# Performance work log

Hardware: AMD Instinct MI355X
Metric: run time of the kernel (lower is better)

## Reference

```python
import jax, jax.numpy as jnp
import numpy as np

NEG_INF = -1e16


def setup_inputs() -> dict:
    key = jax.random.key(0)
    k1, k2, k3 = jax.random.split(key, 3)
    B, N, C, D = 8, 4096, 64, 64
    inputs = jax.random.normal(k1, (B, N, C), dtype=jnp.float32)
    graph = jax.random.randint(k2, (N, N), 0, 2, dtype=jnp.int32)
    # xavier_uniform for Linear weight [D, C]
    limit = float(np.sqrt(6.0 / (C + D)))
    W = jax.random.uniform(k3, (D, C), dtype=jnp.float32, minval=-limit, maxval=limit)
    b = jnp.zeros((D,), dtype=jnp.float32)
    return {"inputs": inputs, "graph": graph, "W": W, "b": b}


def reference(inputs, graph, W, b):
    # h = W(inputs): [B, N, D]
    h = jnp.einsum('bnc,dc->bnd', inputs, W)
    # dense pairwise scores: [B, N, N]
    scores = jnp.einsum('bnd,bmd->bnm', h, h)
    # mask non-edges (graph broadcasts over batch)
    scores = jnp.where(graph[None, :, :] == 0, NEG_INF, scores)
    attention = jax.nn.softmax(scores, axis=2)
    out = jnp.einsum('bnm,bmd->bnd', attention, h) + b
    return out
```

## Files before the change

kernel.cpp:

```cpp
#include <hip/hip_runtime.h>
#include <stdint.h>

typedef _Float16 f16x8 __attribute__((ext_vector_type(8)));
typedef __fp16 half2_t __attribute__((ext_vector_type(2)));
typedef float f32x4 __attribute__((ext_vector_type(4)));

#define LOG2E 1.44269504088896340736f
#define NEGINF (-1e16f)

constexpr int kN = 4096;
constexpr int kD = 64;
constexpr int kB = 8;

__global__ __launch_bounds__(256) void hproj_kernel(const float* __restrict__ x,
                                                    const float* __restrict__ W,
                                                    _Float16* __restrict__ hout,
                                                    _Float16* __restrict__ hTout)
{
    __shared__ float Wt[64][64];
    __shared__ float xs[64][65];

    const int tid = threadIdx.x;
    const int r   = tid >> 2;
    const int c0  = (tid & 3) * 16;

    #pragma unroll
    for (int j = 0; j < 16; j += 4) {
        const float4 v = *(const float4*)(W + r * 64 + c0 + j);
        Wt[c0 + j + 0][r] = v.x;
        Wt[c0 + j + 1][r] = v.y;
        Wt[c0 + j + 2][r] = v.z;
        Wt[c0 + j + 3][r] = v.w;
    }
    const long rowbase = (long)blockIdx.x * 64;
    #pragma unroll
    for (int j = 0; j < 16; j += 4) {
        const float4 v = *(const float4*)(x + (rowbase + r) * 64 + c0 + j);
        xs[r][c0 + j + 0] = v.x;
        xs[r][c0 + j + 1] = v.y;
        xs[r][c0 + j + 2] = v.z;
        xs[r][c0 + j + 3] = v.w;
    }
    __syncthreads();

    const int d0 = (tid & 3) * 16;
    f32x4 acc[4] = {{0.f,0.f,0.f,0.f},{0.f,0.f,0.f,0.f},{0.f,0.f,0.f,0.f},{0.f,0.f,0.f,0.f}};
    #pragma unroll 4
    for (int c = 0; c < 64; ++c) {
        const float xv = xs[r][c];
        const f32x4* wrow = (const f32x4*)&Wt[c][d0];
        #pragma unroll
        for (int k = 0; k < 4; ++k) acc[k] += wrow[k] * xv;
    }
    f16x8 o0, o1;
    #pragma unroll
    for (int j = 0; j < 8; ++j) {
        o0[j] = (_Float16)acc[j >> 2][j & 3];
        o1[j] = (_Float16)acc[2 + (j >> 2)][j & 3];
    }
    *(f16x8*)(hout + (rowbase + r) * 64 + d0)     = o0;
    *(f16x8*)(hout + (rowbase + r) * 64 + d0 + 8) = o1;

    const int bb = blockIdx.x >> 6;
    const int n  = (int)(rowbase + r) & (kN - 1);
    _Float16* hTb = hTout + (long)bb * kD * kN + n;
    #pragma unroll
    for (int j = 0; j < 8; ++j) {
        hTb[(long)(d0 + j) * kN]     = o0[j];
        hTb[(long)(d0 + 8 + j) * kN] = o1[j];
    }
}

__global__ __launch_bounds__(256) void bitpack_kernel(const int* __restrict__ g,
                                                      uint32_t* __restrict__ mw)
{
    const long w = (long)blockIdx.x * 256 + threadIdx.x;
    const int4* p = (const int4*)(g + w * 32);
    uint32_t bits = 0;
    #pragma unroll
    for (int j = 0; j < 8; ++j) {
        const int4 v = p[j];
        bits |= (uint32_t)(v.x != 0) << (j * 4 + 0);
        bits |= (uint32_t)(v.y != 0) << (j * 4 + 1);
        bits |= (uint32_t)(v.z != 0) << (j * 4 + 2);
        bits |= (uint32_t)(v.w != 0) << (j * 4 + 3);
    }
    mw[w] = bits;
}

__global__ __launch_bounds__(256) void masktr_kernel(const uint32_t* __restrict__ mw,
                                                     uint64_t* __restrict__ wmout)
{
    const int tid  = threadIdx.x;
    const int wv   = tid >> 6;
    const int lane = tid & 63;
    const int ll   = lane & 15;
    const int lg   = lane >> 4;
    const int pair = blockIdx.x * 4 + wv;
    const int q16  = pair >> 6;
    const int kv64 = pair & 63;

    const uint2 u = *(const uint2*)(mw + (long)(q16 * 16 + ll) * 128 + kv64 * 2);

    uint64_t Wb[16];
    #pragma unroll
    for (int s = 0; s < 16; ++s) {
        const int t = s >> 2, rr = s & 3;
        const uint32_t word = (t >= 2) ? u.y : u.x;
        const int pos = 8 * lg + 4 * (t & 1) + rr;
        Wb[s] = __ballot(((word >> pos) & 1u) != 0);
    }

    const int s = lane;
    uint64_t a0 = (s & 1) ? Wb[1]  : Wb[0];
    uint64_t a1 = (s & 1) ? Wb[3]  : Wb[2];
    uint64_t a2 = (s & 1) ? Wb[5]  : Wb[4];
    uint64_t a3 = (s & 1) ? Wb[7]  : Wb[6];
    uint64_t a4 = (s & 1) ? Wb[9]  : Wb[8];
    uint64_t a5 = (s & 1) ? Wb[11] : Wb[10];
    uint64_t a6 = (s & 1) ? Wb[13] : Wb[12];
    uint64_t a7 = (s & 1) ? Wb[15] : Wb[14];
    uint64_t b0 = (s & 2) ? a1 : a0;
    uint64_t b1 = (s & 2) ? a3 : a2;
    uint64_t b2 = (s & 2) ? a5 : a4;
    uint64_t b3 = (s & 2) ? a7 : a6;
    uint64_t c0 = (s & 4) ? b1 : b0;
    uint64_t c1 = (s & 4) ? b3 : b2;
    uint64_t v  = (s & 8) ? c1 : c0;
    if (lane < 16) wmout[(long)pair * 16 + lane] = v;
}

__global__ __launch_bounds__(256) void attn_kernel(const _Float16* __restrict__ h,
                                                   const _Float16* __restrict__ hT,
                                                   const uint64_t* __restrict__ wmask,
                                                   const float* __restrict__ bias,
                                                   float* __restrict__ outp,
                                                   float* __restrict__ pO,
                                                   float* __restrict__ pml,
                                                   int kvlen)
{
    __shared__ alignas(16) char Kl[2][8192];
    __shared__ alignas(16) char Vt[2][8192];

    const int b     = blockIdx.y;
    const int split = blockIdx.z;
    const int q0    = blockIdx.x * 64;
    const int tid   = threadIdx.x;
    const int wave  = tid >> 6;
    const int lane  = tid & 63;
    const int lg    = lane >> 4;
    const int ll    = lane & 15;

    const _Float16* hb  = h  + (long)b * kN * kD;
    const _Float16* hTb = hT + (long)b * kD * kN;
    const int kv_base = split * kvlen;
    const int NT      = kvlen / 64;

    const int q = q0 + wave * 16 + ll;
    const f16x8 qf0 = *(const f16x8*)(hb + q * 64 + lg * 8);
    const f16x8 qf1 = *(const f16x8*)(hb + q * 64 + 32 + lg * 8);

    f16x8 vone;
    {
        const _Float16 o = (ll == 0) ? (_Float16)1.0f : (_Float16)0.0f;
        #pragma unroll
        for (int j = 0; j < 8; ++j) vone[j] = o;
    }

    f32x4 Oacc[4] = {{0.f,0.f,0.f,0.f},{0.f,0.f,0.f,0.f},{0.f,0.f,0.f,0.f},{0.f,0.f,0.f,0.f}};
    f32x4 Oacc4 = {0.f, 0.f, 0.f, 0.f};
    float m_run = NEGINF;
    float mm = NEGINF * LOG2E;
    float negv = NEGINF;

    const int sr = tid >> 2;
    const int sc = (tid & 3) * 16;
    const int srp = (sr & 0x23) | ((sr & 0x18) >> 1) | ((sr & 0x4) << 2);

    const int kwA = srp * 128 + ((sc * 2)      ^ ((srp & 7) << 4));
    const int kwB = srp * 128 + ((sc * 2 + 16) ^ ((srp & 7) << 4));
    const int vwA = sr  * 128 + ((sc * 2)      ^ ((sr  & 7) << 4));
    const int vwB = sr  * 128 + ((sc * 2 + 16) ^ ((sr  & 7) << 4));
    const int rb0 = ll * 128 + (((lg * 16))      ^ ((ll & 7) << 4));
    const int rb1 = ll * 128 + (((64 + lg * 16)) ^ ((ll & 7) << 4));

    char* const KB = (char*)Kl;
    char* const VB = (char*)Vt;

    const _Float16* gK = hb  + (long)(kv_base + sr) * 64 + sc;
    const _Float16* gV = hTb + (long)sr * kN + kv_base + sc;

    const int wuni = __builtin_amdgcn_readfirstlane(wave);
    const uint64_t* __restrict__ wmp =
        wmask + ((long)(blockIdx.x * 4 + wuni) * 64 + (kv_base >> 6)) * 16;

    uint64_t wmA[16], wmB[16];
    {
        const f16x8 a0 = *(const f16x8*)(gK);
        const f16x8 a1 = *(const f16x8*)(gK + 8);
        const f16x8 b0 = *(const f16x8*)(gV);
        const f16x8 b1 = *(const f16x8*)(gV + 8);
        *(f16x8*)(KB + kwA) = a0;  *(f16x8*)(KB + kwB) = a1;
        *(f16x8*)(VB + vwA) = b0;  *(f16x8*)(VB + vwB) = b1;
        gK += 64 * 64;  gV += 64;
        #pragma unroll
        for (int s = 0; s < 16; ++s) wmA[s] = wmp[s];
    }

#define TILE_BODY(WMC, WMN, IT, CB, NB)                                          \
    do {                                                                         \
        const int it_ = (IT);                                                    \
        f16x8 nk0{}, nk1{}, nv0{}, nv1{};                                        \
        if (it_ + 1 < NT) {                                                      \
            nk0 = *(const f16x8*)(gK);                                           \
            nk1 = *(const f16x8*)(gK + 8);                                       \
            nv0 = *(const f16x8*)(gV);                                           \
            nv1 = *(const f16x8*)(gV + 8);                                       \
            gK += 64 * 64;  gV += 64;                                            \
            _Pragma("unroll")                                                    \
            for (int s5 = 0; s5 < 16; ++s5) WMN[s5] = wmp[(long)(it_+1)*16 + s5];\
        }                                                                        \
        __syncthreads();                                                         \
        f32x4 S[4];                                                              \
        _Pragma("unroll")                                                        \
        for (int t = 0; t < 4; ++t) {                                            \
            const f16x8 k0 = *(const f16x8*)(KB + (CB) + rb0 + t * 2048);        \
            const f16x8 k1 = *(const f16x8*)(KB + (CB) + rb1 + t * 2048);        \
            f32x4 s = {0.f, 0.f, 0.f, 0.f};                                      \
            s = __builtin_amdgcn_mfma_f32_16x16x32_f16(k0, qf0, s, 0, 0, 0);     \
            s = __builtin_amdgcn_mfma_f32_16x16x32_f16(k1, qf1, s, 0, 0, 0);     \
            S[t] = s;                                                            \
        }                                                                        \
        if (it_ + 1 < NT) {                                                      \
            *(f16x8*)(KB + (NB) + kwA) = nk0;  *(f16x8*)(KB + (NB) + kwB) = nk1; \
            *(f16x8*)(VB + (NB) + vwA) = nv0;  *(f16x8*)(VB + (NB) + vwB) = nv1; \
        }                                                                        \
        _Pragma("unroll")                                                        \
        for (int t = 0; t < 4; ++t) {                                            \
            _Pragma("unroll")                                                    \
            for (int rr = 0; rr < 4; ++rr) {                                     \
                float sv = S[t][rr];                                             \
                asm("v_cndmask_b32 %0, %1, %2, %3"                               \
                    : "=v"(sv) : "v"(negv), "v"(sv), "s"(WMC[t * 4 + rr]));      \
                S[t][rr] = sv;                                                   \
            }                                                                    \
        }                                                                        \
        float mx0 = fmaxf(fmaxf(S[0][0], S[0][1]), fmaxf(S[0][2], S[0][3]));     \
        float mx1 = fmaxf(fmaxf(S[1][0], S[1][1]), fmaxf(S[1][2], S[1][3]));     \
        float mx2 = fmaxf(fmaxf(S[2][0], S[2][1]), fmaxf(S[2][2], S[2][3]));     \
        float mx3 = fmaxf(fmaxf(S[3][0], S[3][1]), fmaxf(S[3][2], S[3][3]));     \
        float mloc = fmaxf(fmaxf(mx0, mx1), fmaxf(mx2, mx3));                    \
        mloc = fmaxf(mloc, __shfl_xor(mloc, 16));                                \
        mloc = fmaxf(mloc, __shfl_xor(mloc, 32));                                \
        if (__any(mloc > m_run + 8.f)) {                                         \
            const float mnew = fmaxf(m_run, mloc);                               \
            const float scl  = __builtin_amdgcn_exp2f((m_run - mnew) * LOG2E);   \
            m_run = mnew;                                                        \
            mm    = mnew * LOG2E;                                                \
            _Pragma("unroll")                                                    \
            for (int dt = 0; dt < 4; ++dt) Oacc[dt] *= scl;                      \
            Oacc4 *= scl;                                                        \
        }                                                                        \
        _Pragma("unroll")                                                        \
        for (int t = 0; t < 4; ++t) {                                            \
            _Pragma("unroll")                                                    \
            for (int rr = 0; rr < 4; ++rr)                                       \
                S[t][rr] = __builtin_amdgcn_exp2f(fmaf(S[t][rr], LOG2E, -mm));   \
        }                                                                        \
        union PF { half2_t hh[4]; f16x8 v; };                                    \
        PF pf1, pf2;                                                             \
        pf1.hh[0] = __builtin_amdgcn_cvt_pkrtz(S[0][0], S[0][1]);                \
        pf1.hh[1] = __builtin_amdgcn_cvt_pkrtz(S[0][2], S[0][3]);                \
        pf1.hh[2] = __builtin_amdgcn_cvt_pkrtz(S[1][0], S[1][1]);                \
        pf1.hh[3] = __builtin_amdgcn_cvt_pkrtz(S[1][2], S[1][3]);                \
        pf2.hh[0] = __builtin_amdgcn_cvt_pkrtz(S[2][0], S[2][1]);                \
        pf2.hh[1] = __builtin_amdgcn_cvt_pkrtz(S[2][2], S[2][3]);                \
        pf2.hh[2] = __builtin_amdgcn_cvt_pkrtz(S[3][0], S[3][1]);                \
        pf2.hh[3] = __builtin_amdgcn_cvt_pkrtz(S[3][2], S[3][3]);                \
        _Pragma("unroll")                                                        \
        for (int dt = 0; dt < 4; ++dt) {                                         \
            const f16x8 v0 = *(const f16x8*)(VB + (CB) + rb0 + dt * 2048);       \
            const f16x8 v1 = *(const f16x8*)(VB + (CB) + rb1 + dt * 2048);       \
            Oacc[dt] = __builtin_amdgcn_mfma_f32_16x16x32_f16(v0, pf1.v, Oacc[dt], 0, 0, 0); \
            Oacc[dt] = __builtin_amdgcn_mfma_f32_16x16x32_f16(v1, pf2.v, Oacc[dt], 0, 0, 0); \
        }                                                                        \
        Oacc4 = __builtin_amdgcn_mfma_f32_16x16x32_f16(vone, pf1.v, Oacc4, 0, 0, 0); \
        Oacc4 = __builtin_amdgcn_mfma_f32_16x16x32_f16(vone, pf2.v, Oacc4, 0, 0, 0); \
    } while (0)

    for (int ith = 0; ith < NT; ith += 2) {
        TILE_BODY(wmA, wmB, ith,     0,    8192);
        TILE_BODY(wmB, wmA, ith + 1, 8192, 0);
    }
#undef TILE_BODY

    const float lsum = __shfl(Oacc4[0], ll, 64);

    if (outp != nullptr) {
        const float inv = 1.0f / lsum;
        #pragma unroll
        for (int dt = 0; dt < 4; ++dt) {
            const int dbase = dt * 16 + lg * 4;
            const f32x4 bv = *(const f32x4*)(bias + dbase);
            f32x4 o;
            #pragma unroll
            for (int rr = 0; rr < 4; ++rr) o[rr] = Oacc[dt][rr] * inv + bv[rr];
            *(f32x4*)(outp + ((long)b * kN + q) * 64 + dbase) = o;
        }
    } else {
        const long srow = (long)split * kB * kN + (long)b * kN + q;
        #pragma unroll
        for (int dt = 0; dt < 4; ++dt) {
            const int dbase = dt * 16 + lg * 4;
            *(f32x4*)(pO + srow * 64 + dbase) = Oacc[dt];
        }
        if (lane < 16) {
            pml[srow * 2 + 0] = m_run;
            pml[srow * 2 + 1] = lsum;
        }
    }
}

__global__ __launch_bounds__(256) void combine_kernel(const float* __restrict__ pO,
                                                      const float* __restrict__ pml,
                                                      const float* __restrict__ bias,
                                                      float* __restrict__ outp,
                                                      int ks)
{
    const long idx = (long)blockIdx.x * 256 + threadIdx.x;
    const long row = idx >> 4;
    const int  d4  = (int)(idx & 15) * 4;

    float M = NEGINF;
    for (int s = 0; s < ks; ++s)
        M = fmaxf(M, pml[((long)s * kB * kN + row) * 2]);

    float L = 0.f;
    f32x4 acc = {0.f, 0.f, 0.f, 0.f};
    for (int s = 0; s < ks; ++s) {
        const long srow = (long)s * kB * kN + row;
        const float m = pml[srow * 2 + 0];
        const float l = pml[srow * 2 + 1];
        const float w = __builtin_amdgcn_exp2f((m - M) * LOG2E);
        L += l * w;
        const f32x4 o = *(const f32x4*)(pO + srow * 64 + d4);
        acc += o * w;
    }
    const float invL = (L > 0.f) ? (1.0f / L) : 0.f;
    const f32x4 bv = *(const f32x4*)(bias + d4);
    *(f32x4*)(outp + row * 64 + d4) = acc * invL + bv;
}

extern "C" void kernel_launch(void* const* d_in, const int* in_sizes, int n_in,
                              void* d_out, int out_size, void* d_ws, size_t ws_size,
                              hipStream_t stream) {
    const float*  x     = (const float*)d_in[0];
    const int*    graph = (const int*)d_in[1];
    const float*  W     = (const float*)d_in[2];
    const float*  bias  = (const float*)d_in[3];
    float*        outp  = (float*)d_out;

    char* ws = (char*)d_ws;
    _Float16* hptr  = (_Float16*)ws;
    uint32_t* mwptr = (uint32_t*)(ws + (4u << 20));
    _Float16* hTptr = (_Float16*)(ws + (6u << 20));
    uint64_t* wmptr = (uint64_t*)(ws + (10u << 20));

    int ks = 1;
    if      (ws_size >= ((size_t)46 << 20)) ks = 4;
    else if (ws_size >= ((size_t)30 << 20)) ks = 2;

    float* pO  = (float*)(ws + (12u << 20));
    float* pml = (float*)(ws + (12u << 20) + (size_t)ks * (8u << 20));

    hproj_kernel<<<dim3(kB * kN / 64), dim3(256), 0, stream>>>(x, W, hptr, hTptr);
    bitpack_kernel<<<dim3(kN * (kN / 32) / 256), dim3(256), 0, stream>>>(graph, mwptr);
    masktr_kernel<<<dim3(256 * 64 / 4), dim3(256), 0, stream>>>(mwptr, wmptr);

    if (ks == 1) {
        attn_kernel<<<dim3(kN / 64, kB, 1), dim3(256), 0, stream>>>(
            hptr, hTptr, wmptr, bias, outp, nullptr, nullptr, kN);
    } else {
        attn_kernel<<<dim3(kN / 64, kB, ks), dim3(256), 0, stream>>>(
            hptr, hTptr, wmptr, bias, nullptr, pO, pml, kN / ks);
        combine_kernel<<<dim3(kB * kN * 16 / 256), dim3(256), 0, stream>>>(
            pO, pml, bias, outp, ks);
    }
}
```

Baseline: 99.12 us.

## Share KV tiles across 8 waves per block and coalesce transposed h writes

The attention kernel now runs 512 threads (8 waves) per block and covers 128 queries, so each K/V tile staged in LDS is reused by twice as many query rows. Each thread now loads half as many fragments per tile. Separately, the projection kernel transposes h through shared memory, so the hT stores become 16-byte vector writes instead of scattered 2-byte stores. In exchange the grid has fewer, larger blocks, which may lower occupancy or hurt load balance, and the split-k grid shrinks.

New measurement: 90.64 us. 8.6% less time.

```diff
diff --git a/kernel.cpp b/kernel.cpp
--- a/kernel.cpp
+++ b/kernel.cpp
@@ -19,6 +19,7 @@
 {
     __shared__ float Wt[64][64];
     __shared__ float xs[64][65];
+    __shared__ _Float16 ht[64][68];
 
     const int tid = threadIdx.x;
     const int r   = tid >> 2;
@@ -61,14 +62,26 @@
     *(f16x8*)(hout + (rowbase + r) * 64 + d0)     = o0;
     *(f16x8*)(hout + (rowbase + r) * 64 + d0 + 8) = o1;
 
+    #pragma unroll
+    for (int j = 0; j < 8; ++j) {
+        ht[r][d0 + j]     = o0[j];
+        ht[r][d0 + 8 + j] = o1[j];
+    }
+    __syncthreads();
+
     const int bb = blockIdx.x >> 6;
-    const int n  = (int)(rowbase + r) & (kN - 1);
-    _Float16* hTb = hTout + (long)bb * kD * kN + n;
+    const int n0 = (int)(rowbase & (kN - 1));
+    const int dr = tid >> 2;
+    const int c4 = (tid & 3) * 16;
+    f16x8 t0, t1;
     #pragma unroll
     for (int j = 0; j < 8; ++j) {
-        hTb[(long)(d0 + j) * kN]     = o0[j];
-        hTb[(long)(d0 + 8 + j) * kN] = o1[j];
-    }
+        t0[j] = ht[c4 + j][dr];
+        t1[j] = ht[c4 + 8 + j][dr];
+    }
+    _Float16* dst = hTout + (long)bb * kD * kN + (long)dr * kN + n0 + c4;
+    *(f16x8*)(dst)     = t0;
+    *(f16x8*)(dst + 8) = t1;
 }
 
 __global__ __launch_bounds__(256) void bitpack_kernel(const int* __restrict__ g,
@@ -130,7 +143,7 @@
     if (lane < 16) wmout[(long)pair * 16 + lane] = v;
 }
 
-__global__ __launch_bounds__(256) void attn_kernel(const _Float16* __restrict__ h,
+__global__ __launch_bounds__(512) void attn_kernel(const _Float16* __restrict__ h,
                                                    const _Float16* __restrict__ hT,
                                                    const uint64_t* __restrict__ wmask,
                                                    const float* __restrict__ bias,
@@ -144,7 +157,7 @@
 
     const int b     = blockIdx.y;
     const int split = blockIdx.z;
-    const int q0    = blockIdx.x * 64;
+    const int q0    = blockIdx.x * 128;
     const int tid   = threadIdx.x;
     const int wave  = tid >> 6;
     const int lane  = tid & 63;
@@ -173,35 +186,31 @@
     float mm = NEGINF * LOG2E;
     float negv = NEGINF;
 
-    const int sr = tid >> 2;
-    const int sc = (tid & 3) * 16;
+    const int sr  = tid >> 3;
+    const int sc8 = (tid & 7) * 8;
     const int srp = (sr & 0x23) | ((sr & 0x18) >> 1) | ((sr & 0x4) << 2);
 
-    const int kwA = srp * 128 + ((sc * 2)      ^ ((srp & 7) << 4));
-    const int kwB = srp * 128 + ((sc * 2 + 16) ^ ((srp & 7) << 4));
-    const int vwA = sr  * 128 + ((sc * 2)      ^ ((sr  & 7) << 4));
-    const int vwB = sr  * 128 + ((sc * 2 + 16) ^ ((sr  & 7) << 4));
+    const int kw = srp * 128 + ((sc8 * 2) ^ ((srp & 7) << 4));
+    const int vw = sr  * 128 + ((sc8 * 2) ^ ((sr  & 7) << 4));
     const int rb0 = ll * 128 + (((lg * 16))      ^ ((ll & 7) << 4));
     const int rb1 = ll * 128 + (((64 + lg * 16)) ^ ((ll & 7) << 4));
 
     char* const KB = (char*)Kl;
     char* const VB = (char*)Vt;
 
-    const _Float16* gK = hb  + (long)(kv_base + sr) * 64 + sc;
-    const _Float16* gV = hTb + (long)sr * kN + kv_base + sc;
+    const _Float16* gK = hb  + (long)(kv_base + sr) * 64 + sc8;
+    const _Float16* gV = hTb + (long)sr * kN + kv_base + sc8;
 
     const int wuni = __builtin_amdgcn_readfirstlane(wave);
     const uint64_t* __restrict__ wmp =
-        wmask + ((long)(blockIdx.x * 4 + wuni) * 64 + (kv_base >> 6)) * 16;
+        wmask + ((long)(blockIdx.x * 8 + wuni) * 64 + (kv_base >> 6)) * 16;
 
     uint64_t wmA[16], wmB[16];
     {
         const f16x8 a0 = *(const f16x8*)(gK);
-        const f16x8 a1 = *(const f16x8*)(gK + 8);
         const f16x8 b0 = *(const f16x8*)(gV);
-        const f16x8 b1 = *(const f16x8*)(gV + 8);
-        *(f16x8*)(KB + kwA) = a0;  *(f16x8*)(KB + kwB) = a1;
-        *(f16x8*)(VB + vwA) = b0;  *(f16x8*)(VB + vwB) = b1;
+        *(f16x8*)(KB + kw) = a0;
+        *(f16x8*)(VB + vw) = b0;
         gK += 64 * 64;  gV += 64;
         #pragma unroll
         for (int s = 0; s < 16; ++s) wmA[s] = wmp[s];
@@ -210,12 +219,10 @@
 #define TILE_BODY(WMC, WMN, IT, CB, NB)                                          \
     do {                                                                         \
         const int it_ = (IT);                                                    \
-        f16x8 nk0{}, nk1{}, nv0{}, nv1{};                                        \
+        f16x8 nk0{}, nv0{};                                                      \
         if (it_ + 1 < NT) {                                                      \
             nk0 = *(const f16x8*)(gK);                                           \
-            nk1 = *(const f16x8*)(gK + 8);                                       \
             nv0 = *(const f16x8*)(gV);                                           \
-            nv1 = *(const f16x8*)(gV + 8);                                       \
             gK += 64 * 64;  gV += 64;                                            \
             _Pragma("unroll")                                                    \
             for (int s5 = 0; s5 < 16; ++s5) WMN[s5] = wmp[(long)(it_+1)*16 + s5];\
@@ -232,8 +239,8 @@
             S[t] = s;                                                            \
         }                                                                        \
         if (it_ + 1 < NT) {                                                      \
-            *(f16x8*)(KB + (NB) + kwA) = nk0;  *(f16x8*)(KB + (NB) + kwB) = nk1; \
-            *(f16x8*)(VB + (NB) + vwA) = nv0;  *(f16x8*)(VB + (NB) + vwB) = nv1; \
+            *(f16x8*)(KB + (NB) + kw) = nk0;                                     \
+            *(f16x8*)(VB + (NB) + vw) = nv0;                                     \
         }                                                                        \
         _Pragma("unroll")                                                        \
         for (int t = 0; t < 4; ++t) {                                            \
@@ -378,10 +385,10 @@
     masktr_kernel<<<dim3(256 * 64 / 4), dim3(256), 0, stream>>>(mwptr, wmptr);
 
     if (ks == 1) {
-        attn_kernel<<<dim3(kN / 64, kB, 1), dim3(256), 0, stream>>>(
+        attn_kernel<<<dim3(kN / 128, kB, 1), dim3(512), 0, stream>>>(
             hptr, hTptr, wmptr, bias, outp, nullptr, nullptr, kN);
     } else {
-        attn_kernel<<<dim3(kN / 64, kB, ks), dim3(256), 0, stream>>>(
+        attn_kernel<<<dim3(kN / 128, kB, ks), dim3(512), 0, stream>>>(
             hptr, hTptr, wmptr, bias, nullptr, pO, pml, kN / ks);
         combine_kernel<<<dim3(kB * kN * 16 / 256), dim3(256), 0, stream>>>(
             pO, pml, bias, outp, ks);
```
